# Performance work log

Hardware: AMD Instinct MI355X
Metric: run time of the kernel (lower is better)

The kernel has to match this reference:

```python
import jax, jax.numpy as jnp
import numpy as np
import math

HEADS = 32
GROUPS = 8
HEAD_DIM = 64
HIDDEN = 2048
B, S = 2, 2048


def _rope(x, freqs_cis):
    # x: (..., S, head_dim); freqs_cis: (S, head_dim) -> interleaved cos/sin pattern
    x_even = x[..., ::2]
    x_odd = x[..., 1::2]
    cos = freqs_cis[..., ::2]
    sin = freqs_cis[..., 1::2]
    r_even = x_even * cos - x_odd * sin
    r_odd = x_even * sin + x_odd * cos
    return jnp.stack([r_even, r_odd], axis=-1).reshape(x.shape)


def setup_inputs() -> dict:
    key = jax.random.key(0)
    ks = jax.random.split(key, 12)
    scale = 1.0 / math.sqrt(HIDDEN)
    x = jax.random.normal(ks[0], (B, S, HIDDEN), dtype=jnp.float32)
    freqs_cis = jax.random.uniform(ks[1], (S, HEAD_DIM), dtype=jnp.float32)
    causal = jnp.tril(jnp.ones((S, S), dtype=bool))
    mask = jnp.where(causal, 0.0, -1e9).astype(jnp.float32)
    kv_dims = HEAD_DIM * GROUPS
    wq = jax.random.normal(ks[2], (HIDDEN, HIDDEN), jnp.float32) * scale
    bq = jnp.zeros((HIDDEN,), jnp.float32)
    wk = jax.random.normal(ks[3], (kv_dims, HIDDEN), jnp.float32) * scale
    bk = jnp.zeros((kv_dims,), jnp.float32)
    wv = jax.random.normal(ks[4], (kv_dims, HIDDEN), jnp.float32) * scale
    bv = jnp.zeros((kv_dims,), jnp.float32)
    wo = jax.random.normal(ks[5], (HIDDEN, HIDDEN), jnp.float32) * scale
    bo = jnp.zeros((HIDDEN,), jnp.float32)
    return dict(x=x, freqs_cis=freqs_cis, mask=mask, wq=wq, bq=bq,
                wk=wk, bk=bk, wv=wv, bv=bv, wo=wo, bo=bo)


def reference(x, freqs_cis, mask, wq, bq, wk, bk, wv, bv, wo, bo):
    b, s, h = x.shape
    rep = HEADS // GROUPS
    q = x @ wq.T + bq                      # (B,S,H)
    k = x @ wk.T + bk                      # (B,S,G*hd)
    v = x @ wv.T + bv
    q = q.reshape(b, s, HEADS, HEAD_DIM).transpose(0, 2, 1, 3)   # (B,Hh,S,hd)
    k = k.reshape(b, s, GROUPS, HEAD_DIM).transpose(0, 2, 1, 3)  # (B,G,S,hd)
    v = v.reshape(b, s, GROUPS, HEAD_DIM).transpose(0, 2, 1, 3)
    q = _rope(q, freqs_cis)
    k = _rope(k, freqs_cis)
    # GQA: group q heads instead of materially repeating K/V
    qg = q.reshape(b, GROUPS, rep, s, HEAD_DIM)
    scores = jnp.einsum('bgrsd,bgtd->bgrst', qg, k) / math.sqrt(HEAD_DIM)
    scores = scores + mask                 # broadcast (S,S)
    attn = jax.nn.softmax(scores, axis=-1)
    out = jnp.einsum('bgrst,bgtd->bgrsd', attn, v)
    out = out.reshape(b, HEADS, s, HEAD_DIM).transpose(0, 2, 1, 3).reshape(b, s, h)
    return out @ wo.T + bo
```

## Files before the change

kernel.cpp:

```cpp
#include <hip/hip_runtime.h>

#define S_LEN 2048
#define HID   2048
#define NQH   32
#define NKV   8
#define HD    64

#define BM 128
#define BN 128
#define BK 32

typedef __bf16 bf16x8 __attribute__((ext_vector_type(8)));
typedef __bf16 bf16x4 __attribute__((ext_vector_type(4)));
typedef float  f32x4  __attribute__((ext_vector_type(4)));

#define MFMA16(a, b, c) __builtin_amdgcn_mfma_f32_16x16x32_bf16(a, b, c, 0, 0, 0)

__device__ __forceinline__ void async_copy16(const void* g, void* l) {
  __builtin_amdgcn_global_load_lds(
      (const __attribute__((address_space(1))) unsigned int*)g,
      (__attribute__((address_space(3))) unsigned int*)l, 16, 0, 0);
}

__device__ __forceinline__ unsigned cvtpk_bf16(float lo, float hi) {
  unsigned r;
  asm("v_cvt_pk_bf16_f32 %0, %1, %2" : "=v"(r) : "v"(lo), "v"(hi));
  return r;
}

__global__ void cast_all_k(const float* __restrict__ x,  const float* __restrict__ wq,
                           const float* __restrict__ wk, const float* __restrict__ wv,
                           const float* __restrict__ wo,
                           __bf16* __restrict__ xb,  __bf16* __restrict__ wqb,
                           __bf16* __restrict__ wkb, __bf16* __restrict__ wvb,
                           __bf16* __restrict__ wob) {
  int bid = blockIdx.x;
  const float* in; __bf16* out; int base;
  if (bid < 8192)       { in = x;  out = xb;  base = bid; }
  else if (bid < 12288) { in = wq; out = wqb; base = bid - 8192; }
  else if (bid < 13312) { in = wk; out = wkb; base = bid - 12288; }
  else if (bid < 14336) { in = wv; out = wvb; base = bid - 13312; }
  else                  { in = wo; out = wob; base = bid - 14336; }
  int i = (base * 256 + threadIdx.x) * 4;
  float4 v = *(const float4*)(in + i);
  bf16x4 o;
  o[0] = (__bf16)v.x; o[1] = (__bf16)v.y; o[2] = (__bf16)v.z; o[3] = (__bf16)v.w;
  *(bf16x4*)(out + i) = o;
}

__device__ __forceinline__ void gemm_pipe(const __bf16* __restrict__ A,
                                          const __bf16* __restrict__ B,
                                          int m0, int n0, int K,
                                          __bf16 (&As)[3][BM][BK],
                                          __bf16 (&Bs)[3][BN][BK],
                                          f32x4 (&acc)[4][4]) {
  const int tid = threadIdx.x, wave = tid >> 6, lane = tid & 63;
  const int l15 = lane & 15, quad = lane >> 4;
  const int wr = wave >> 1, wc = wave & 1;

  const int srow   = tid >> 2;
  const int schunk = (tid & 3) ^ ((tid >> 3) & 3);
  const __bf16* ga = A + (size_t)(m0 + srow) * K + schunk * 8;
  const __bf16* gb = B + (size_t)(n0 + srow) * K + schunk * 8;

  const int co = (quad ^ ((l15 >> 1) & 3)) * 8;

  const int NT = K / BK;

#define STAGE(st, kt) do {                                              \
    async_copy16(ga + (kt),                  &As[st][wave * 16][0]);    \
    async_copy16(ga + (kt) + (size_t)64 * K, &As[st][64 + wave * 16][0]); \
    async_copy16(gb + (kt),                  &Bs[st][wave * 16][0]);    \
    async_copy16(gb + (kt) + (size_t)64 * K, &Bs[st][64 + wave * 16][0]); \
  } while (0)

  STAGE(0, 0);
  STAGE(1, BK);

  int s = 0;
#pragma unroll 1
  for (int t = 0; t < NT; t++) {
    if (t + 1 < NT) asm volatile("s_waitcnt vmcnt(4)" ::: "memory");
    else            asm volatile("s_waitcnt vmcnt(0)" ::: "memory");
    __builtin_amdgcn_s_barrier();
    asm volatile("" ::: "memory");

    if (t + 2 < NT) {
      int s2 = s + 2; if (s2 >= 3) s2 -= 3;
      STAGE(s2, (t + 2) * BK);
    }

    const __bf16* a0 = &As[s][wr * 64][0];
    const __bf16* b0 = &Bs[s][wc * 64][0];
    bf16x8 af[4], bfr[4];
#pragma unroll
    for (int mt = 0; mt < 4; mt++)
      af[mt] = *(const bf16x8*)(a0 + (mt * 16 + l15) * BK + co);
#pragma unroll
    for (int nt = 0; nt < 4; nt++)
      bfr[nt] = *(const bf16x8*)(b0 + (nt * 16 + l15) * BK + co);

    __builtin_amdgcn_s_setprio(1);
#pragma unroll
    for (int mt = 0; mt < 4; mt++)
#pragma unroll
      for (int nt = 0; nt < 4; nt++)
        acc[mt][nt] = MFMA16(af[mt], bfr[nt], acc[mt][nt]);
    __builtin_amdgcn_s_setprio(0);

    s = s + 1; if (s >= 3) s -= 3;
  }
#undef STAGE
}

__global__ __launch_bounds__(256, 3) void gemm_qkv_k(const __bf16* __restrict__ xb,
    const __bf16* __restrict__ wqb, const __bf16* __restrict__ wkb, const __bf16* __restrict__ wvb,
    const float* __restrict__ bq, const float* __restrict__ bk, const float* __restrict__ bv,
    const float* __restrict__ fr,
    __bf16* __restrict__ Qb, __bf16* __restrict__ Kb, __bf16* __restrict__ Vt) {
  __shared__ __align__(16) __bf16 As[3][BM][BK];
  __shared__ __align__(16) __bf16 Bs[3][BN][BK];
  const int by = blockIdx.y;
  const int m0 = blockIdx.x * BM;
  const __bf16* B; const float* bias; int n0;
  int mode;
  if (by < 16)      { B = wqb; bias = bq; n0 = by * 128;        mode = 0; }
  else if (by < 20) { B = wkb; bias = bk; n0 = (by - 16) * 128; mode = 1; }
  else              { B = wvb; bias = bv; n0 = (by - 20) * 128; mode = 2; }

  f32x4 acc[4][4] = {};
  gemm_pipe(xb, B, m0, n0, HID, As, Bs, acc);

  const int tid = threadIdx.x, wave = tid >> 6, lane = tid & 63;
  const int l15 = lane & 15, quad = lane >> 4;
  const int wr = wave >> 1, wc = wave & 1;

  if (mode == 2) {
#pragma unroll
    for (int nt = 0; nt < 4; nt++) {
      int col = n0 + wc * 64 + nt * 16 + l15;
      int g = col >> 6, d = col & 63;
      float bv2 = bias[col];
#pragma unroll
      for (int mt = 0; mt < 4; mt++) {
        int row = m0 + wr * 64 + mt * 16 + quad * 4;
        int b = row >> 11, sI = row & 2047;
        bf16x4 o;
#pragma unroll
        for (int r = 0; r < 4; r++) o[r] = (__bf16)(acc[mt][nt][r] + bv2);
        *(bf16x4*)(Vt + (((size_t)(b * NKV + g) * HD + d)) * S_LEN + sI) = o;
      }
    }
  } else if (mode == 0) {
#pragma unroll
    for (int nt = 0; nt < 4; nt++) {
      int col = n0 + wc * 64 + nt * 16 + l15;
      float bv2 = bias[col];
#pragma unroll
      for (int mt = 0; mt < 4; mt++) {
        int row = m0 + wr * 64 + mt * 16 + quad * 4;
#pragma unroll
        for (int r = 0; r < 4; r++)
          Qb[(size_t)(row + r) * HID + col] = (__bf16)(acc[mt][nt][r] + bv2);
      }
    }
  } else {
    const int dpar = l15 & 1;
#pragma unroll
    for (int nt = 0; nt < 4; nt++) {
      int col = n0 + wc * 64 + nt * 16 + l15;
      int d = col & 63;
      float bv2 = bias[col];
#pragma unroll
      for (int mt = 0; mt < 4; mt++) {
        int row = m0 + wr * 64 + mt * 16 + quad * 4;
        int sI = row & 2047;
#pragma unroll
        for (int r = 0; r < 4; r++) {
          float v = acc[mt][nt][r] + bv2;
          float p = __shfl_xor(v, 1, 64);
          float f = fr[(size_t)(sI + r) * HD + d];
          float fp = __shfl_xor(f, 1, 64);
          float o = dpar ? (p * f + v * fp) : (v * f - p * fp);
          Kb[(size_t)(row + r) * 512 + col] = (__bf16)o;
        }
      }
    }
  }
}

__global__ __launch_bounds__(256, 3) void gemm_out_k(const __bf16* __restrict__ A,
    const __bf16* __restrict__ Bw, const float* __restrict__ bias, float* __restrict__ C) {
  __shared__ __align__(16) __bf16 As[3][BM][BK];
  __shared__ __align__(16) __bf16 Bs[3][BN][BK];
  const int m0 = blockIdx.x * BM, n0 = blockIdx.y * BN;
  f32x4 acc[4][4] = {};
  gemm_pipe(A, Bw, m0, n0, HID, As, Bs, acc);
  const int tid = threadIdx.x, wave = tid >> 6, lane = tid & 63;
  const int l15 = lane & 15, quad = lane >> 4;
  const int wr = wave >> 1, wc = wave & 1;
#pragma unroll
  for (int nt = 0; nt < 4; nt++) {
    int col = n0 + wc * 64 + nt * 16 + l15;
    float bv = bias[col];
#pragma unroll
    for (int mt = 0; mt < 4; mt++) {
      int row = m0 + wr * 64 + mt * 16 + quad * 4;
#pragma unroll
      for (int r = 0; r < 4; r++)
        C[(size_t)(row + r) * HID + col] = acc[mt][nt][r] + bv;
    }
  }
}

__device__ __forceinline__ void rope8(bf16x8& q, const float* f, float sc) {
  float4 fa = *(const float4*)f;
  float4 fb = *(const float4*)(f + 4);
  float e, o;
  e = (float)q[0]; o = (float)q[1];
  q[0] = (__bf16)((e * fa.x - o * fa.y) * sc);
  q[1] = (__bf16)((e * fa.y + o * fa.x) * sc);
  e = (float)q[2]; o = (float)q[3];
  q[2] = (__bf16)((e * fa.z - o * fa.w) * sc);
  q[3] = (__bf16)((e * fa.w + o * fa.z) * sc);
  e = (float)q[4]; o = (float)q[5];
  q[4] = (__bf16)((e * fb.x - o * fb.y) * sc);
  q[5] = (__bf16)((e * fb.y + o * fb.x) * sc);
  e = (float)q[6]; o = (float)q[7];
  q[6] = (__bf16)((e * fb.z - o * fb.w) * sc);
  q[7] = (__bf16)((e * fb.w + o * fb.z) * sc);
}

__global__ __launch_bounds__(256, 4) void flash_k(const __bf16* __restrict__ Q,
                                                  const __bf16* __restrict__ K,
                                                  const __bf16* __restrict__ Vt,
                                                  const float* __restrict__ fr,
                                                  __bf16* __restrict__ O) {
  __shared__ __align__(64) __bf16 Ksm[2][64][64];
  __shared__ __align__(64) __bf16 Vsm[2][64][64];
  const int tid = threadIdx.x;
  const int wave = tid >> 6, lane = tid & 63;
  const int l15 = lane & 15, quad = lane >> 4;
  const int bh = blockIdx.x;
  const int b = bh >> 5, h = bh & 31, g = h >> 2;

  const int srow = tid >> 2, sc = (tid & 3) * 16;
  const int r7 = srow & 7;
  const int w0 = (((sc >> 3))     ^ r7) * 8;
  const int w1 = (((sc >> 3) + 1) ^ r7) * 8;

  const char* kbp = (const char*)&Ksm[0][0][0];
  const char* vbp = (const char*)&Vsm[0][0][0];

  const int x7  = l15 & 7;
  const int sig = 8 * ((l15 >> 2) & 1) + 4 * (l15 >> 3) + (l15 & 3);
  const int s7  = sig & 7;
  int krK[2], krV[2];
#pragma unroll
  for (int ks = 0; ks < 2; ks++) {
    krK[ks] = sig * 128 + (((ks * 4 + quad) ^ s7) * 16);
    krV[ks] = l15 * 128 + (((ks * 4 + quad) ^ x7) * 16);
  }
  const int kvb = 8 * (quad & 1) + 4 * (quad >> 1);

  bf16x8 ones;
#pragma unroll
  for (int j = 0; j < 8; j++) ones[j] = (__bf16)1.0f;

  const __bf16* kbase = K + ((size_t)b * S_LEN + srow) * (NKV * HD) + g * HD + sc;
  const __bf16* vbase = Vt + (((size_t)b * NKV + g) * HD + srow) * S_LEN + sc;
  const float QSC = 0.125f * 1.44269504f;
  const int KSTEP = 64 * NKV * HD;

#pragma unroll 1
  for (int half = 0; half < 2; half++) {
    const int qt = half ? (31 - (int)blockIdx.y) : (int)blockIdx.y;
    const int wq0 = qt * 64 + wave * 16;

    const __bf16* qp = Q + ((size_t)(b * S_LEN + wq0 + l15)) * HID + h * HD + quad * 8;
    bf16x8 qf0 = *(const bf16x8*)qp;
    bf16x8 qf1 = *(const bf16x8*)(qp + 32);
    const float* fq = fr + (size_t)(wq0 + l15) * HD + quad * 8;
    rope8(qf0, fq, QSC);
    rope8(qf1, fq + 32, QSC);

    f32x4 acc[4] = {};
    f32x4 accs = {};

    const __bf16* kp = kbase;
    const __bf16* vp = vbase;
    uint4 k0 = *(const uint4*)kp, k1 = *(const uint4*)(kp + 8);
    uint4 v0 = *(const uint4*)vp, v1 = *(const uint4*)(vp + 8);
    *(uint4*)&Ksm[0][srow][w0] = k0;
    *(uint4*)&Ksm[0][srow][w1] = k1;
    *(uint4*)&Vsm[0][srow][w0] = v0;
    *(uint4*)&Vsm[0][srow][w1] = v1;
    if (qt > 0) {
      kp += KSTEP;  vp += 64;
      k0 = *(const uint4*)kp; k1 = *(const uint4*)(kp + 8);
      v0 = *(const uint4*)vp; v1 = *(const uint4*)(vp + 8);
    }
    __syncthreads();

#pragma unroll 1
    for (int t = 0; t <= qt; t++) {
      const int cur = t & 1;
      const int kv0 = t * 64;

      if (t < qt) {
        *(uint4*)&Ksm[cur ^ 1][srow][w0] = k0;
        *(uint4*)&Ksm[cur ^ 1][srow][w1] = k1;
        *(uint4*)&Vsm[cur ^ 1][srow][w0] = v0;
        *(uint4*)&Vsm[cur ^ 1][srow][w1] = v1;
        if (t + 2 <= qt) {
          kp += KSTEP;  vp += 64;
          k0 = *(const uint4*)kp; k1 = *(const uint4*)(kp + 8);
          v0 = *(const uint4*)vp; v1 = *(const uint4*)(vp + 8);
        }
      }

      if (kv0 <= wq0 + 15) {
        const int cb = cur * 8192;
        bf16x8 kf[2][4];
#pragma unroll
        for (int ks = 0; ks < 2; ks++)
#pragma unroll
          for (int nt = 0; nt < 4; nt++)
            kf[ks][nt] = *(const bf16x8*)(kbp + cb + krK[ks] + nt * 2048);

        f32x4 sacc[4] = {};
#pragma unroll
        for (int nt = 0; nt < 4; nt++) {
          sacc[nt] = MFMA16(kf[0][nt], qf0, sacc[nt]);
          sacc[nt] = MFMA16(kf[1][nt], qf1, sacc[nt]);
        }

        const bool domask = (kv0 + 63 > wq0);
        const int md = wq0 + l15 - kv0 - kvb;
        unsigned W[4][2];
#pragma unroll
        for (int nt = 0; nt < 4; nt++) {
          f32x4 pv;
#pragma unroll
          for (int r = 0; r < 4; r++) pv[r] = __builtin_exp2f(sacc[nt][r]);
          if (domask) {
#pragma unroll
            for (int r = 0; r < 4; r++)
              if (nt * 16 + r > md) pv[r] = 0.f;
          }
          W[nt][0] = cvtpk_bf16(pv[0], pv[1]);
          W[nt][1] = cvtpk_bf16(pv[2], pv[3]);
        }

#pragma unroll
        for (int ks = 0; ks < 2; ks++) {
          unsigned a0 = W[2 * ks][0], b0 = W[2 * ks + 1][0];
          unsigned a1 = W[2 * ks][1], b1 = W[2 * ks + 1][1];
          asm("v_permlane32_swap_b32 %0, %1" : "+v"(a0), "+v"(b0));
          asm("v_permlane32_swap_b32 %0, %1" : "+v"(a1), "+v"(b1));
          union { unsigned u[4]; bf16x8 v; } pk;
          pk.u[0] = a0; pk.u[1] = a1; pk.u[2] = b0; pk.u[3] = b1;
          bf16x8 pf = pk.v;

          bf16x8 vf[4];
#pragma unroll
          for (int nt = 0; nt < 4; nt++)
            vf[nt] = *(const bf16x8*)(vbp + cb + krV[ks] + nt * 2048);
          accs = MFMA16(pf, ones, accs);
#pragma unroll
          for (int nt = 0; nt < 4; nt++)
            acc[nt] = MFMA16(pf, vf[nt], acc[nt]);
        }
      }

      __syncthreads();
    }

    __bf16* op = O + ((size_t)(b * S_LEN + wq0 + quad * 4)) * HID + h * HD;
    float inv[4];
#pragma unroll
    for (int r = 0; r < 4; r++) inv[r] = 1.f / accs[r];
#pragma unroll
    for (int nt = 0; nt < 4; nt++)
#pragma unroll
      for (int r = 0; r < 4; r++)
        op[(size_t)r * HID + nt * 16 + l15] = (__bf16)(acc[nt][r] * inv[r]);
  }
}

extern "C" void kernel_launch(void* const* d_in, const int* in_sizes, int n_in,
                              void* d_out, int out_size, void* d_ws, size_t ws_size,
                              hipStream_t stream) {
  (void)in_sizes; (void)n_in; (void)out_size; (void)ws_size;
  const float* x  = (const float*)d_in[0];
  const float* fr = (const float*)d_in[1];
  const float* wq = (const float*)d_in[3];
  const float* bq = (const float*)d_in[4];
  const float* wk = (const float*)d_in[5];
  const float* bk = (const float*)d_in[6];
  const float* wv = (const float*)d_in[7];
  const float* bv = (const float*)d_in[8];
  const float* wo = (const float*)d_in[9];
  const float* bo = (const float*)d_in[10];
  float* out = (float*)d_out;
  char* ws = (char*)d_ws;

  __bf16* xb  = (__bf16*)(ws);
  __bf16* wqb = (__bf16*)(ws + ((size_t)16 << 20));
  __bf16* wkb = (__bf16*)(ws + ((size_t)24 << 20));
  __bf16* wvb = (__bf16*)(ws + ((size_t)26 << 20));
  __bf16* wob = (__bf16*)(ws + ((size_t)28 << 20));
  __bf16* Qb  = (__bf16*)(ws + ((size_t)36 << 20));
  __bf16* Kb  = (__bf16*)(ws + ((size_t)52 << 20));
  __bf16* Vtb = (__bf16*)(ws + ((size_t)60 << 20));
  __bf16* Ab  = (__bf16*)(ws + ((size_t)64 << 20));

  cast_all_k<<<18432, 256, 0, stream>>>(x, wq, wk, wv, wo, xb, wqb, wkb, wvb, wob);

  gemm_qkv_k<<<dim3(32, 24), 256, 0, stream>>>(xb, wqb, wkb, wvb, bq, bk, bv, fr, Qb, Kb, Vtb);

  flash_k<<<dim3(64, 16), 256, 0, stream>>>(Qb, Kb, Vtb, fr, Ab);

  gemm_out_k<<<dim3(32, 16), 256, 0, stream>>>(Ab, wob, bo, out);
}
```

Measured before the change: 309.1 us.

## Process two 64-row query tiles per flash block to reuse K/V loads

Each flash attention block now handles 128 query rows (two 64-row sub-tiles A and B) instead of 64. Every K/V tile staged in LDS is used by both sub-tiles, which halves global and LDS K/V traffic per query row. The grid is halved accordingly and launch bounds drop to 2 blocks per CU, because twice as many accumulators raise register pressure. The cost is fewer blocks for occupancy and latency hiding, plus coarser causal balancing.

```diff
diff --git a/kernel.cpp b/kernel.cpp
--- a/kernel.cpp
+++ b/kernel.cpp
@@ -231,7 +231,7 @@
   q[7] = (__bf16)((e * fb.w + o * fb.z) * sc);
 }
 
-__global__ __launch_bounds__(256, 4) void flash_k(const __bf16* __restrict__ Q,
+__global__ __launch_bounds__(256, 2) void flash_k(const __bf16* __restrict__ Q,
                                                   const __bf16* __restrict__ K,
                                                   const __bf16* __restrict__ Vt,
                                                   const float* __restrict__ fr,
@@ -274,18 +274,25 @@
 
 #pragma unroll 1
   for (int half = 0; half < 2; half++) {
-    const int qt = half ? (31 - (int)blockIdx.y) : (int)blockIdx.y;
-    const int wq0 = qt * 64 + wave * 16;
-
-    const __bf16* qp = Q + ((size_t)(b * S_LEN + wq0 + l15)) * HID + h * HD + quad * 8;
-    bf16x8 qf0 = *(const bf16x8*)qp;
-    bf16x8 qf1 = *(const bf16x8*)(qp + 32);
-    const float* fq = fr + (size_t)(wq0 + l15) * HD + quad * 8;
-    rope8(qf0, fq, QSC);
-    rope8(qf1, fq + 32, QSC);
-
-    f32x4 acc[4] = {};
-    f32x4 accs = {};
+    const int qt = half ? (15 - (int)blockIdx.y) : (int)blockIdx.y;
+    const int NT = 2 * qt + 2;
+    const int wq0 = qt * 128 + wave * 16;
+
+    const __bf16* qpA = Q + ((size_t)(b * S_LEN + wq0 + l15)) * HID + h * HD + quad * 8;
+    const __bf16* qpB = qpA + (size_t)64 * HID;
+    bf16x8 qfA0 = *(const bf16x8*)qpA;
+    bf16x8 qfA1 = *(const bf16x8*)(qpA + 32);
+    bf16x8 qfB0 = *(const bf16x8*)qpB;
+    bf16x8 qfB1 = *(const bf16x8*)(qpB + 32);
+    const float* fqA = fr + (size_t)(wq0 + l15) * HD + quad * 8;
+    const float* fqB = fqA + (size_t)64 * HD;
+    rope8(qfA0, fqA, QSC);
+    rope8(qfA1, fqA + 32, QSC);
+    rope8(qfB0, fqB, QSC);
+    rope8(qfB1, fqB + 32, QSC);
+
+    f32x4 accA[4] = {}, accB[4] = {};
+    f32x4 accsA = {}, accsB = {};
 
     const __bf16* kp = kbase;
     const __bf16* vp = vbase;
@@ -295,49 +302,49 @@
     *(uint4*)&Ksm[0][srow][w1] = k1;
     *(uint4*)&Vsm[0][srow][w0] = v0;
     *(uint4*)&Vsm[0][srow][w1] = v1;
-    if (qt > 0) {
-      kp += KSTEP;  vp += 64;
-      k0 = *(const uint4*)kp; k1 = *(const uint4*)(kp + 8);
-      v0 = *(const uint4*)vp; v1 = *(const uint4*)(vp + 8);
-    }
+    kp += KSTEP;  vp += 64;
+    k0 = *(const uint4*)kp; k1 = *(const uint4*)(kp + 8);
+    v0 = *(const uint4*)vp; v1 = *(const uint4*)(vp + 8);
     __syncthreads();
 
 #pragma unroll 1
-    for (int t = 0; t <= qt; t++) {
+    for (int t = 0; t < NT; t++) {
       const int cur = t & 1;
       const int kv0 = t * 64;
 
-      if (t < qt) {
+      if (t + 1 < NT) {
         *(uint4*)&Ksm[cur ^ 1][srow][w0] = k0;
         *(uint4*)&Ksm[cur ^ 1][srow][w1] = k1;
         *(uint4*)&Vsm[cur ^ 1][srow][w0] = v0;
         *(uint4*)&Vsm[cur ^ 1][srow][w1] = v1;
-        if (t + 2 <= qt) {
+        if (t + 2 < NT) {
           kp += KSTEP;  vp += 64;
           k0 = *(const uint4*)kp; k1 = *(const uint4*)(kp + 8);
           v0 = *(const uint4*)vp; v1 = *(const uint4*)(vp + 8);
         }
       }
 
-      if (kv0 <= wq0 + 15) {
-        const int cb = cur * 8192;
-        bf16x8 kf[2][4];
-#pragma unroll
-        for (int ks = 0; ks < 2; ks++)
-#pragma unroll
-          for (int nt = 0; nt < 4; nt++)
-            kf[ks][nt] = *(const bf16x8*)(kbp + cb + krK[ks] + nt * 2048);
-
+      const bool actA = (kv0 <= wq0 + 15);
+      const int cb = cur * 8192;
+
+      bf16x8 kf[2][4];
+#pragma unroll
+      for (int ks = 0; ks < 2; ks++)
+#pragma unroll
+        for (int nt = 0; nt < 4; nt++)
+          kf[ks][nt] = *(const bf16x8*)(kbp + cb + krK[ks] + nt * 2048);
+
+      unsigned WB[4][2];
+      {
         f32x4 sacc[4] = {};
 #pragma unroll
         for (int nt = 0; nt < 4; nt++) {
-          sacc[nt] = MFMA16(kf[0][nt], qf0, sacc[nt]);
-          sacc[nt] = MFMA16(kf[1][nt], qf1, sacc[nt]);
-        }
-
-        const bool domask = (kv0 + 63 > wq0);
-        const int md = wq0 + l15 - kv0 - kvb;
-        unsigned W[4][2];
+          sacc[nt] = MFMA16(kf[0][nt], qfB0, sacc[nt]);
+          sacc[nt] = MFMA16(kf[1][nt], qfB1, sacc[nt]);
+        }
+        const int wq0B = wq0 + 64;
+        const bool domask = (kv0 + 63 > wq0B);
+        const int md = wq0B + l15 - kv0 - kvb;
 #pragma unroll
         for (int nt = 0; nt < 4; nt++) {
           f32x4 pv;
@@ -348,43 +355,85 @@
             for (int r = 0; r < 4; r++)
               if (nt * 16 + r > md) pv[r] = 0.f;
           }
-          W[nt][0] = cvtpk_bf16(pv[0], pv[1]);
-          W[nt][1] = cvtpk_bf16(pv[2], pv[3]);
-        }
-
-#pragma unroll
-        for (int ks = 0; ks < 2; ks++) {
-          unsigned a0 = W[2 * ks][0], b0 = W[2 * ks + 1][0];
-          unsigned a1 = W[2 * ks][1], b1 = W[2 * ks + 1][1];
+          WB[nt][0] = cvtpk_bf16(pv[0], pv[1]);
+          WB[nt][1] = cvtpk_bf16(pv[2], pv[3]);
+        }
+      }
+      unsigned WA[4][2];
+      if (actA) {
+        f32x4 sacc[4] = {};
+#pragma unroll
+        for (int nt = 0; nt < 4; nt++) {
+          sacc[nt] = MFMA16(kf[0][nt], qfA0, sacc[nt]);
+          sacc[nt] = MFMA16(kf[1][nt], qfA1, sacc[nt]);
+        }
+        const bool domask = (kv0 + 63 > wq0);
+        const int md = wq0 + l15 - kv0 - kvb;
+#pragma unroll
+        for (int nt = 0; nt < 4; nt++) {
+          f32x4 pv;
+#pragma unroll
+          for (int r = 0; r < 4; r++) pv[r] = __builtin_exp2f(sacc[nt][r]);
+          if (domask) {
+#pragma unroll
+            for (int r = 0; r < 4; r++)
+              if (nt * 16 + r > md) pv[r] = 0.f;
+          }
+          WA[nt][0] = cvtpk_bf16(pv[0], pv[1]);
+          WA[nt][1] = cvtpk_bf16(pv[2], pv[3]);
+        }
+      }
+
+#pragma unroll
+      for (int ks = 0; ks < 2; ks++) {
+        bf16x8 vf[4];
+#pragma unroll
+        for (int nt = 0; nt < 4; nt++)
+          vf[nt] = *(const bf16x8*)(vbp + cb + krV[ks] + nt * 2048);
+
+        {
+          unsigned a0 = WB[2 * ks][0], b0 = WB[2 * ks + 1][0];
+          unsigned a1 = WB[2 * ks][1], b1 = WB[2 * ks + 1][1];
           asm("v_permlane32_swap_b32 %0, %1" : "+v"(a0), "+v"(b0));
           asm("v_permlane32_swap_b32 %0, %1" : "+v"(a1), "+v"(b1));
           union { unsigned u[4]; bf16x8 v; } pk;
           pk.u[0] = a0; pk.u[1] = a1; pk.u[2] = b0; pk.u[3] = b1;
           bf16x8 pf = pk.v;
-
-          bf16x8 vf[4];
+          accsB = MFMA16(pf, ones, accsB);
 #pragma unroll
           for (int nt = 0; nt < 4; nt++)
-            vf[nt] = *(const bf16x8*)(vbp + cb + krV[ks] + nt * 2048);
-          accs = MFMA16(pf, ones, accs);
+            accB[nt] = MFMA16(pf, vf[nt], accB[nt]);
+        }
+        if (actA) {
+          unsigned a0 = WA[2 * ks][0], b0 = WA[2 * ks + 1][0];
+          unsigned a1 = WA[2 * ks][1], b1 = WA[2 * ks + 1][1];
+          asm("v_permlane32_swap_b32 %0, %1" : "+v"(a0), "+v"(b0));
+          asm("v_permlane32_swap_b32 %0, %1" : "+v"(a1), "+v"(b1));
+          union { unsigned u[4]; bf16x8 v; } pk;
+          pk.u[0] = a0; pk.u[1] = a1; pk.u[2] = b0; pk.u[3] = b1;
+          bf16x8 pf = pk.v;
+          accsA = MFMA16(pf, ones, accsA);
 #pragma unroll
           for (int nt = 0; nt < 4; nt++)
-            acc[nt] = MFMA16(pf, vf[nt], acc[nt]);
+            accA[nt] = MFMA16(pf, vf[nt], accA[nt]);
         }
       }
 
       __syncthreads();
     }
 
-    __bf16* op = O + ((size_t)(b * S_LEN + wq0 + quad * 4)) * HID + h * HD;
-    float inv[4];
-#pragma unroll
-    for (int r = 0; r < 4; r++) inv[r] = 1.f / accs[r];
+    __bf16* opA = O + ((size_t)(b * S_LEN + wq0 + quad * 4)) * HID + h * HD;
+    __bf16* opB = opA + (size_t)64 * HID;
+    float invA[4], invB[4];
+#pragma unroll
+    for (int r = 0; r < 4; r++) { invA[r] = 1.f / accsA[r]; invB[r] = 1.f / accsB[r]; }
 #pragma unroll
     for (int nt = 0; nt < 4; nt++)
 #pragma unroll
-      for (int r = 0; r < 4; r++)
-        op[(size_t)r * HID + nt * 16 + l15] = (__bf16)(acc[nt][r] * inv[r]);
+      for (int r = 0; r < 4; r++) {
+        opA[(size_t)r * HID + nt * 16 + l15] = (__bf16)(accA[nt][r] * invA[r]);
+        opB[(size_t)r * HID + nt * 16 + l15] = (__bf16)(accB[nt][r] * invB[r]);
+      }
   }
 }
 
@@ -419,7 +468,7 @@
 
   gemm_qkv_k<<<dim3(32, 24), 256, 0, stream>>>(xb, wqb, wkb, wvb, bq, bk, bv, fr, Qb, Kb, Vtb);
 
-  flash_k<<<dim3(64, 16), 256, 0, stream>>>(Qb, Kb, Vtb, fr, Ab);
+  flash_k<<<dim3(64, 8), 256, 0, stream>>>(Qb, Kb, Vtb, fr, Ab);
 
   gemm_out_k<<<dim3(32, 16), 256, 0, stream>>>(Ab, wob, bo, out);
 }
```

Result: no change. 308.3 us (-0.2%).
